# Kernel tuning notes

Hardware: AMD Instinct MI355X
Metric: run time of the kernel (lower is better)

The kernel has to match this reference:

```python
import jax, jax.numpy as jnp
import numpy as np

P_SCALE = 5.0
Q_SCALE = 0.3
EPS = 1e-06
NORM_EPS = 1e-12


def stack3x3_same(img):
    """im2col for 3x3 kernel, 'same' zero padding, stride 1.
    img: (B,H,W,C) -> (B,H,W,9,C), tap order row-major (dy,dx) in {-1,0,1}^2,
    matching the TF stack3x3 ordering with clip=0, pad=1."""
    B, H, W, C = img.shape
    padded = jnp.pad(img, ((0, 0), (1, 1), (1, 1), (0, 0)))
    taps = [padded[:, dy:dy + H, dx:dx + W, :] for dy in range(3) for dx in range(3)]
    return jnp.stack(taps, axis=3)


def setup_inputs() -> dict:
    key = jax.random.key(0)
    k1, k2 = jax.random.split(key)
    B, H, W, C = 32, 64, 64, 64
    n_kernels, ksize = 128, 3
    inputs = jax.random.normal(k1, (B, H, W, C), dtype=jnp.float32)
    # glorot-uniform-ish weight, shape (1, C*k*k, n_kernels)
    fan_in = C * ksize * ksize
    limit = np.sqrt(6.0 / (fan_in + n_kernels)).astype(np.float32)
    w = jax.random.uniform(k2, (1, fan_in, n_kernels), dtype=jnp.float32,
                           minval=-limit, maxval=limit)
    p = jnp.full((n_kernels,), 0.7 * P_SCALE, dtype=jnp.float32)
    q = jnp.full((1,), 1.0 * Q_SCALE, dtype=jnp.float32)
    return {"inputs": inputs, "w": w, "p": p, "q": q}


def reference(inputs, w, p, q):
    B, H, W, C = inputs.shape
    n_kernels = w.shape[-1]
    ksq = w.shape[1] // C  # kernel_size^2 = 9

    # im2col: (B, H*W, C*9), tap-major flatten (matches tf stack axis=3 + reshape)
    x = stack3x3_same(inputs).reshape(B, H * W, ksq * C)

    p_eff = jnp.exp(p / P_SCALE)            # (n_kernels,)
    q_eff = jnp.exp(-q / Q_SCALE)           # (1,)

    # L2 norms (sqrt of clamped square-sum), matching l2_normal
    x_norm = jnp.sqrt(jnp.maximum(jnp.sum(x * x, axis=2, keepdims=True), NORM_EPS)) + q_eff
    w_norm = jnp.sqrt(jnp.maximum(jnp.sum(w * w, axis=1, keepdims=True), NORM_EPS))

    # cosine-similarity matmul: (B, HW, K) x (1, K, N) -> (B, HW, N)
    sim = jnp.einsum('bsk,kn->bsn', x / x_norm, (w / w_norm)[0])

    # sharpened rescaling: sign(x) * (|x| + eps)^p
    out = jnp.sign(sim) * jnp.power(jnp.abs(sim) + EPS, p_eff)
    return out.reshape(B, H, W, n_kernels)
```

## Files before the change

### kernel.cpp

```cpp
#include <hip/hip_runtime.h>
#include <hip/hip_bf16.h>


typedef short bf16x8 __attribute__((ext_vector_type(8)));
typedef float f32x4 __attribute__((ext_vector_type(4)));

__device__ __forceinline__ unsigned short f2bf(float f) {
    union { float f; unsigned int u; } v; v.f = f;
    unsigned int u = v.u;
    unsigned int r = (u + 0x7fffu + ((u >> 16) & 1u)) >> 16;
    return (unsigned short)r;
}

__global__ void prep_w_kernel(const float* __restrict__ w,
                              unsigned short* __restrict__ wn2) {
    const int n = blockIdx.x;
    const int lane = threadIdx.x;
    float vals[9];
    float s = 0.f;
#pragma unroll
    for (int i = 0; i < 9; ++i) {
        float v = w[(i * 64 + lane) * 128 + n];
        vals[i] = v;
        s += v * v;
    }
#pragma unroll
    for (int off = 1; off < 64; off <<= 1) s += __shfl_xor(s, off);
    const float inv = 1.0f / sqrtf(fmaxf(s, 1e-12f));
    const int kc = lane >> 5, koff = lane & 31;
#pragma unroll
    for (int i = 0; i < 9; ++i)
        wn2[((i * 2 + kc) * 128 + n) * 32 + koff] = f2bf(vals[i] * inv);
}

#define OBLD 68

__global__ __launch_bounds__(256, 4) void cossim_main(
    const float* __restrict__ in, const unsigned short* __restrict__ wn,
    const float* __restrict__ p, const float* __restrict__ q,
    float* __restrict__ out) {
    __shared__ __align__(16) unsigned char smemRaw[4 * 66 * 72 * 2];
    unsigned short* A = reinterpret_cast<unsigned short*>(smemRaw);
    float* OB = reinterpret_cast<float*>(smemRaw);
    __shared__ float rcsum[256];
    __shared__ float xni[128];
    __shared__ float pfs[64];

    const int tid = (int)threadIdx.x;
    const int l = ((int)blockIdx.x & 7) * 256 + ((int)blockIdx.x >> 3);
    const int sp = l >> 1, nh = l & 1;
    const int b = sp >> 5, y0 = (sp & 31) * 2;

    if (tid < 64) pfs[tid] = expf(p[nh * 64 + tid] * 0.2f);

    {
        const int r = tid >> 6;
        const int col = tid & 63;
        const int row = y0 + r - 1;
        unsigned short* dst = &A[(r * 66 + col + 1) * 72];
        float s = 0.f;
        if ((unsigned)row < 64u) {
            const float4* src = reinterpret_cast<const float4*>(
                in + (size_t)b * 262144 + row * 4096 + col * 64);
#pragma unroll
            for (int it = 0; it < 8; ++it) {
                float4 v0 = src[2 * it];
                float4 v1 = src[2 * it + 1];
                s += v0.x * v0.x + v0.y * v0.y + v0.z * v0.z + v0.w * v0.w;
                s += v1.x * v1.x + v1.y * v1.y + v1.z * v1.z + v1.w * v1.w;
                union { float f; unsigned u; } ux, uy, uz, uw;
                uint4 pk;
                ux.f = v0.x; uy.f = v0.y; uz.f = v0.z; uw.f = v0.w;
                pk.x = __builtin_amdgcn_perm(uy.u + 0x8000u, ux.u + 0x8000u, 0x07060302u);
                pk.y = __builtin_amdgcn_perm(uw.u + 0x8000u, uz.u + 0x8000u, 0x07060302u);
                ux.f = v1.x; uy.f = v1.y; uz.f = v1.z; uw.f = v1.w;
                pk.z = __builtin_amdgcn_perm(uy.u + 0x8000u, ux.u + 0x8000u, 0x07060302u);
                pk.w = __builtin_amdgcn_perm(uw.u + 0x8000u, uz.u + 0x8000u, 0x07060302u);
                *reinterpret_cast<uint4*>(dst + it * 8) = pk;
            }
        } else {
            uint4 z; z.x = z.y = z.z = z.w = 0u;
#pragma unroll
            for (int it = 0; it < 8; ++it)
                *reinterpret_cast<uint4*>(dst + it * 8) = z;
        }
        rcsum[tid] = s;
    }
    if (tid < 64) {
        const int r = tid >> 4, side = (tid >> 3) & 1, ch = (tid & 7) * 8;
        uint4 z; z.x = z.y = z.z = z.w = 0u;
        *reinterpret_cast<uint4*>(&A[(r * 66 + side * 65) * 72 + ch]) = z;
    }
    __syncthreads();

    if (tid < 128) {
        const int ry = tid >> 6, x = tid & 63;
        const float qe = expf(q[0] * (-1.0f / 0.3f));
        float s = 0.f;
#pragma unroll
        for (int dy = 0; dy < 3; ++dy) {
            const float* rs = &rcsum[(ry + dy) * 64];
            if (x > 0) s += rs[x - 1];
            s += rs[x];
            if (x < 63) s += rs[x + 1];
        }
        xni[tid] = 1.0f / (sqrtf(fmaxf(s, 1e-12f)) + qe);
    }
    __syncthreads();

    const int wv = tid >> 6, lane = tid & 63;
    const int lr = lane & 15, lg = lane >> 4;
    const int wm = wv >> 1, wq = wv & 1;
    f32x4 acc[4][2] = {};
    const unsigned short* wB = wn + (nh * 64 + wq * 32 + lr) * 32 + lg * 8;

    bf16x8 bc0 = *reinterpret_cast<const bf16x8*>(wB);
    bf16x8 bc1 = *reinterpret_cast<const bf16x8*>(wB + 512);

#pragma unroll
    for (int s = 0; s < 18; ++s) {
        bf16x8 bn0, bn1;
        if (s + 1 < 18) {
            const unsigned short* wt = wB + (s + 1) * 4096;
            bn0 = *reinterpret_cast<const bf16x8*>(wt);
            bn1 = *reinterpret_cast<const bf16x8*>(wt + 512);
        }
        const int dy = s / 6, dx = (s >> 1) % 3, kc = s & 1;
#pragma unroll
        for (int mf = 0; mf < 4; ++mf) {
            const unsigned short* ap =
                &A[((wm + dy) * 66 + mf * 16 + lr + dx) * 72 + kc * 32 + lg * 8];
            bf16x8 av = *reinterpret_cast<const bf16x8*>(ap);
            acc[mf][0] = __builtin_amdgcn_mfma_f32_16x16x32_bf16(av, bc0, acc[mf][0], 0, 0, 0);
            acc[mf][1] = __builtin_amdgcn_mfma_f32_16x16x32_bf16(av, bc1, acc[mf][1], 0, 0, 0);
        }
        bc0 = bn0; bc1 = bn1;
    }
    __syncthreads();

    const float* pf = pfs;
#pragma unroll
    for (int mf = 0; mf < 4; ++mf) {
#pragma unroll
        for (int i = 0; i < 4; ++i) {
            const int pix = wm * 64 + mf * 16 + lg * 4 + i;
            const float xn = xni[pix];
#pragma unroll
            for (int nf = 0; nf < 2; ++nf) {
                const int nl = wq * 32 + nf * 16 + lr;
                float sim = acc[mf][nf][i] * xn;
                float aa = fabsf(sim) + 1e-6f;
                float r = exp2f(pf[nl] * log2f(aa));
                OB[pix * OBLD + nl] = copysignf(r, sim);
            }
        }
    }
    __syncthreads();

#pragma unroll
    for (int j = 0; j < 8; ++j) {
        const int f = tid + 256 * j;
        const int px = f >> 4, c = f & 15;
        float4 v = *reinterpret_cast<const float4*>(&OB[px * OBLD + c * 4]);
        const int row = y0 + (px >> 6), col = px & 63;
        *reinterpret_cast<float4*>(
            out + ((size_t)((b * 64 + row) * 64 + col)) * 128 + nh * 64 + c * 4) = v;
    }
}

extern "C" void kernel_launch(void* const* d_in, const int* in_sizes, int n_in,
                              void* d_out, int out_size, void* d_ws, size_t ws_size,
                              hipStream_t stream) {
    (void)in_sizes; (void)n_in; (void)out_size; (void)ws_size;
    const float* in = (const float*)d_in[0];
    const float* w  = (const float*)d_in[1];
    const float* p  = (const float*)d_in[2];
    const float* q  = (const float*)d_in[3];
    float* out = (float*)d_out;
    unsigned short* wn = (unsigned short*)d_ws;

    prep_w_kernel<<<128, 64, 0, stream>>>(w, wn);
    cossim_main<<<2048, 256, 0, stream>>>(in, wn, p, q, out);
}
```

Measured before the change: 50.54 us.

## Switch to 32x32x16 MFMA tiles and store results directly from registers

Replaces the 16x16x32 bf16 MFMA tiling with 32x32x16 MFMAs, so each wave covers a 64-pixel by 32-channel tile with two 16-element accumulators. The A/B fragment indexing and the weight reads are adjusted to match. The epilogue no longer stages output through shared memory behind two barriers. Each lane now computes its channel's exponent and writes scalar floats straight to global memory. This removes LDS round-trips and synchronisation, but the global stores become 4-byte writes strided by 512 bytes per lane instead of coalesced float4 writes.

Measured after the change: 48.64 us. 1.04x faster.

```diff
diff --git a/kernel.cpp b/kernel.cpp
--- a/kernel.cpp
+++ b/kernel.cpp
@@ -3,7 +3,7 @@
 
 
 typedef short bf16x8 __attribute__((ext_vector_type(8)));
-typedef float f32x4 __attribute__((ext_vector_type(4)));
+typedef float f32x16 __attribute__((ext_vector_type(16)));
 
 __device__ __forceinline__ unsigned short f2bf(float f) {
     union { float f; unsigned int u; } v; v.f = f;
@@ -33,25 +33,18 @@
         wn2[((i * 2 + kc) * 128 + n) * 32 + koff] = f2bf(vals[i] * inv);
 }
 
-#define OBLD 68
-
 __global__ __launch_bounds__(256, 4) void cossim_main(
     const float* __restrict__ in, const unsigned short* __restrict__ wn,
     const float* __restrict__ p, const float* __restrict__ q,
     float* __restrict__ out) {
-    __shared__ __align__(16) unsigned char smemRaw[4 * 66 * 72 * 2];
-    unsigned short* A = reinterpret_cast<unsigned short*>(smemRaw);
-    float* OB = reinterpret_cast<float*>(smemRaw);
+    __shared__ unsigned short A[4 * 66 * 72];
     __shared__ float rcsum[256];
     __shared__ float xni[128];
-    __shared__ float pfs[64];
 
     const int tid = (int)threadIdx.x;
     const int l = ((int)blockIdx.x & 7) * 256 + ((int)blockIdx.x >> 3);
     const int sp = l >> 1, nh = l & 1;
     const int b = sp >> 5, y0 = (sp & 31) * 2;
-
-    if (tid < 64) pfs[tid] = expf(p[nh * 64 + tid] * 0.2f);
 
     {
         const int r = tid >> 6;
@@ -109,13 +102,14 @@
     __syncthreads();
 
     const int wv = tid >> 6, lane = tid & 63;
-    const int lr = lane & 15, lg = lane >> 4;
-    const int wm = wv >> 1, wq = wv & 1;
-    f32x4 acc[4][2] = {};
-    const unsigned short* wB = wn + (nh * 64 + wq * 32 + lr) * 32 + lg * 8;
+    const int ln31 = lane & 31, khi = lane >> 5;
+    const int rt = wv >> 1;
+    const int tn = wv & 1;
+    f32x16 acc0 = {}, acc1 = {};
+    const unsigned short* wB = wn + (nh * 64 + tn * 32 + ln31) * 32 + khi * 8;
 
     bf16x8 bc0 = *reinterpret_cast<const bf16x8*>(wB);
-    bf16x8 bc1 = *reinterpret_cast<const bf16x8*>(wB + 512);
+    bf16x8 bc1 = *reinterpret_cast<const bf16x8*>(wB + 16);
 
 #pragma unroll
     for (int s = 0; s < 18; ++s) {
@@ -123,48 +117,37 @@
         if (s + 1 < 18) {
             const unsigned short* wt = wB + (s + 1) * 4096;
             bn0 = *reinterpret_cast<const bf16x8*>(wt);
-            bn1 = *reinterpret_cast<const bf16x8*>(wt + 512);
+            bn1 = *reinterpret_cast<const bf16x8*>(wt + 16);
         }
         const int dy = s / 6, dx = (s >> 1) % 3, kc = s & 1;
-#pragma unroll
-        for (int mf = 0; mf < 4; ++mf) {
-            const unsigned short* ap =
-                &A[((wm + dy) * 66 + mf * 16 + lr + dx) * 72 + kc * 32 + lg * 8];
-            bf16x8 av = *reinterpret_cast<const bf16x8*>(ap);
-            acc[mf][0] = __builtin_amdgcn_mfma_f32_16x16x32_bf16(av, bc0, acc[mf][0], 0, 0, 0);
-            acc[mf][1] = __builtin_amdgcn_mfma_f32_16x16x32_bf16(av, bc1, acc[mf][1], 0, 0, 0);
-        }
+        const unsigned short* arow =
+            &A[((rt + dy) * 66 + ln31 + dx) * 72 + kc * 32 + khi * 8];
+        bf16x8 a00 = *reinterpret_cast<const bf16x8*>(arow);
+        bf16x8 a01 = *reinterpret_cast<const bf16x8*>(arow + 16);
+        bf16x8 a10 = *reinterpret_cast<const bf16x8*>(arow + 32 * 72);
+        bf16x8 a11 = *reinterpret_cast<const bf16x8*>(arow + 32 * 72 + 16);
+        acc0 = __builtin_amdgcn_mfma_f32_32x32x16_bf16(a00, bc0, acc0, 0, 0, 0);
+        acc1 = __builtin_amdgcn_mfma_f32_32x32x16_bf16(a10, bc0, acc1, 0, 0, 0);
+        acc0 = __builtin_amdgcn_mfma_f32_32x32x16_bf16(a01, bc1, acc0, 0, 0, 0);
+        acc1 = __builtin_amdgcn_mfma_f32_32x32x16_bf16(a11, bc1, acc1, 0, 0, 0);
         bc0 = bn0; bc1 = bn1;
     }
-    __syncthreads();
 
-    const float* pf = pfs;
+    const int n = nh * 64 + tn * 32 + ln31;
+    const float pn = expf(p[n] * 0.2f);
+    float* orow = out + ((size_t)(b * 64 + y0 + rt) * 64) * 128 + n;
 #pragma unroll
-    for (int mf = 0; mf < 4; ++mf) {
+    for (int tm = 0; tm < 2; ++tm) {
+        const f32x16& av = tm == 0 ? acc0 : acc1;
 #pragma unroll
-        for (int i = 0; i < 4; ++i) {
-            const int pix = wm * 64 + mf * 16 + lg * 4 + i;
-            const float xn = xni[pix];
-#pragma unroll
-            for (int nf = 0; nf < 2; ++nf) {
-                const int nl = wq * 32 + nf * 16 + lr;
-                float sim = acc[mf][nf][i] * xn;
-                float aa = fabsf(sim) + 1e-6f;
-                float r = exp2f(pf[nl] * log2f(aa));
-                OB[pix * OBLD + nl] = copysignf(r, sim);
-            }
+        for (int r = 0; r < 16; ++r) {
+            const int px = tm * 32 + (r & 3) + 8 * (r >> 2) + 4 * khi;
+            float sim = av[r] * xni[rt * 64 + px];
+            float aa = fabsf(sim) + 1e-6f;
+            float rr = exp2f(pn * log2f(aa));
+            orow[(size_t)px * 128] = copysignf(rr, sim);
+            orow += 0;
         }
-    }
-    __syncthreads();
-
-#pragma unroll
-    for (int j = 0; j < 8; ++j) {
-        const int f = tid + 256 * j;
-        const int px = f >> 4, c = f & 15;
-        float4 v = *reinterpret_cast<const float4*>(&OB[px * OBLD + c * 4]);
-        const int row = y0 + (px >> 6), col = px & 63;
-        *reinterpret_cast<float4*>(
-            out + ((size_t)((b * 64 + row) * 64 + col)) * 128 + nh * 64 + c * 4) = v;
     }
 }
 
```
